# Optimization experiments

Measured on AMD Instinct MI355X. Metric: run time of the kernel, lower is better.

## Reference

```python
import jax, jax.numpy as jnp
import numpy as np
from jax import lax

P = 2048
HIDDEN = 512
NUM_STEPS = 15
BATCH = 8192
SLOPE = 25.0  # snntorch surrogate.fast_sigmoid default slope


@jax.custom_vjp
def spike_fn(x):
    # Heaviside forward, fast-sigmoid surrogate backward.
    return (x > 0).astype(x.dtype)

def _spike_fwd(x):
    return spike_fn(x), x

def _spike_bwd(x, g):
    return (g / (SLOPE * jnp.abs(x) + 1.0) ** 2,)

spike_fn.defvjp(_spike_fwd, _spike_bwd)


def setup_inputs() -> dict:
    key = jax.random.key(0)
    ks = jax.random.split(key, 6)
    x = jax.random.randint(ks[0], (BATCH, 2), 0, P)
    embed = jax.random.normal(ks[1], (P, HIDDEN), dtype=jnp.float32)
    # Linear weights stored [in, out] (transpose of torch convention, same math)
    W1 = jax.random.normal(ks[2], (2 * HIDDEN, HIDDEN), dtype=jnp.float32) * (1.0 / np.sqrt(2 * HIDDEN))
    b1 = jnp.zeros((HIDDEN,), dtype=jnp.float32)
    W2 = jax.random.normal(ks[3], (HIDDEN, P), dtype=jnp.float32) * (1.0 / np.sqrt(HIDDEN))
    b2 = jnp.zeros((P,), dtype=jnp.float32)
    beta1 = jnp.float32(0.9)
    thr1 = jnp.float32(1.0)
    beta2 = jnp.float32(0.9)
    thr2 = jnp.float32(1.0)
    return {"x": x, "embed": embed, "W1": W1, "b1": b1, "W2": W2, "b2": b2,
            "beta1": beta1, "thr1": thr1, "beta2": beta2, "thr2": thr2}


def reference(x, embed, W1, b1, W2, b2, beta1, thr1, beta2, thr2):
    # clamp params as in the torch no-grad block (identity at init values)
    beta1 = jnp.clip(beta1, 0.1, 0.9)
    beta2 = jnp.clip(beta2, 0.1, 0.9)
    thr1 = jnp.clip(thr1, 0.1, None)
    thr2 = jnp.clip(thr2, 0.1, None)

    emb = embed[x].reshape(x.shape[0], -1)          # [B, 2*hidden]
    cur1 = emb @ W1 + b1                            # constant across steps

    mem1_0 = jnp.zeros((x.shape[0], HIDDEN), dtype=jnp.float32)
    mem2_0 = jnp.zeros((x.shape[0], P), dtype=jnp.float32)

    def step(carry, _):
        mem1, mem2 = carry
        # snntorch Leaky, reset_mechanism='subtract': reset from PREVIOUS mem, detached
        reset1 = lax.stop_gradient((mem1 - thr1 > 0).astype(mem1.dtype))
        mem1 = beta1 * mem1 + cur1 - reset1 * thr1
        spk1 = spike_fn(mem1 - thr1)
        cur2 = spk1 @ W2 + b2
        # lif2 has reset_mechanism='none'
        mem2 = beta2 * mem2 + cur2
        return (mem1, mem2), None

    (mem1, mem2), _ = lax.scan(step, (mem1_0, mem2_0), None, length=NUM_STEPS)
    return mem2  # output = last mem2
```

## Files before the change

### kernel.cpp

```cpp
#include <hip/hip_runtime.h>
#include <hip/hip_bf16.h>
#include <stdint.h>

typedef float    f32x4 __attribute__((ext_vector_type(4)));
typedef _Float16 f16x4 __attribute__((ext_vector_type(4)));
typedef _Float16 f16x8 __attribute__((ext_vector_type(8)));

#define NSTEPS 15

__global__ __launch_bounds__(256) void prep_kernel(
    const float* __restrict__ embed, const float* __restrict__ W1,
    const float* __restrict__ W2,
    _Float16* __restrict__ Ap, _Float16* __restrict__ Btp,
    _Float16* __restrict__ W2T)
{
  __shared__ _Float16 sh[2][64][72];
  const int b = blockIdx.x;
  const int t = threadIdx.x;

  if (b < 1024) {
    const int i  = b * 256 + t;
    const int m  = i >> 7;
    const int k4 = (i & 127) * 4;
    f32x4 v = *(const f32x4*)&embed[(size_t)m * 512 + k4];
    f16x4 h0, h1;
#pragma unroll
    for (int j = 0; j < 4; ++j) {
      h0[j] = (_Float16)v[j];
      h1[j] = (_Float16)(v[j] - (float)h0[j]);
    }
    _Float16* r = Ap + (size_t)m * 1024 + k4;
    *(f16x4*)(r)       = h0;
    *(f16x4*)(r + 512) = h1;
  } else if (b < 1152) {
    const int idx = b - 1024;
    const int n0 = (idx & 7) * 64;
    const int k0 = ((idx >> 3) & 7) * 64;
    const int z  = idx >> 6;
    const int kk = t >> 4;
    const int n4 = (t & 15) * 4;
#pragma unroll
    for (int i = 0; i < 4; ++i) {
      f32x4 v = *(const f32x4*)&W1[(size_t)(z * 512 + k0 + kk + i * 16) * 512 + n0 + n4];
#pragma unroll
      for (int j = 0; j < 4; ++j) {
        float s = v[j] * 64.0f;
        _Float16 hi = (_Float16)s;
        sh[0][n4 + j][kk + i * 16] = hi;
        sh[1][n4 + j][kk + i * 16] = (_Float16)(s - (float)hi);
      }
    }
    __syncthreads();
#pragma unroll
    for (int i = 0; i < 2; ++i) {
      const int nn = (t >> 3) + i * 32;
      const int k8 = (t & 7) * 8;
      _Float16* r = Btp + (size_t)(z * 512 + n0 + nn) * 1024 + k0 + k8;
      *(uint4*)(r)       = *(const uint4*)&sh[0][nn][k8];
      *(uint4*)(r + 512) = *(const uint4*)&sh[1][nn][k8];
    }
  } else {
    const int idx = b - 1152;
    const int n0 = (idx & 31) * 64;
    const int k0 = (idx >> 5) * 64;
    const int kk = t >> 4;
    const int n4 = (t & 15) * 4;
#pragma unroll
    for (int i = 0; i < 4; ++i) {
      f32x4 v = *(const f32x4*)&W2[(size_t)(k0 + kk + i * 16) * 2048 + n0 + n4];
#pragma unroll
      for (int j = 0; j < 4; ++j) sh[0][n4 + j][kk + i * 16] = (_Float16)v[j];
    }
    __syncthreads();
#pragma unroll
    for (int i = 0; i < 2; ++i) {
      const int nn = (t >> 3) + i * 32;
      const int k8 = (t & 7) * 8;
      *(uint4*)&W2T[(size_t)(n0 + nn) * 512 + k0 + k8] = *(const uint4*)&sh[0][nn][k8];
    }
  }
}

__device__ __forceinline__ void gld_lds16(const void* g, void* l) {
  __builtin_amdgcn_global_load_lds(
      (const __attribute__((address_space(1))) uint32_t*)g,
      (__attribute__((address_space(3))) uint32_t*)l, 16, 0, 0);
}

__device__ __forceinline__ void g1_stage(
    const _Float16* __restrict__ Ap, const _Float16* __restrict__ Btp,
    char* lds, int m0, int n0, int wave, int lane, int tile)
{
  const int vk0  = tile * 64;
  const int acol = (vk0 < 1024) ? vk0 : vk0 - 1024;
  const int bcol = (vk0 < 1024) ? (vk0 & 511) : vk0 - 512;
  char* lb = lds + (tile % 3) * 16384;
#pragma unroll
  for (int i = 0; i < 2; ++i) {
    const int ob  = (wave * 2 + i) * 1024;
    const int o   = ob + lane * 16;
    const int row = o >> 7;
    const int c   = ((o >> 4) & 7) ^ (row & 7);
    gld_lds16(Ap + ((size_t)(m0 + row) * 1024 + acol + c * 8), lb + ob);
  }
#pragma unroll
  for (int i = 0; i < 2; ++i) {
    const int ob  = (wave * 2 + i) * 1024;
    const int o   = ob + lane * 16;
    const int row = o >> 7;
    const int c   = ((o >> 4) & 7) ^ (row & 7);
    gld_lds16(Btp + ((size_t)(n0 + row) * 1024 + bcol + c * 8), lb + 8192 + ob);
  }
}

__global__ __launch_bounds__(256) void gemm1_kernel(
    const _Float16* __restrict__ Ap,
    const _Float16* __restrict__ Btp,
    float* __restrict__ T)
{
  __shared__ __align__(16) char lds[3 * 16384];

  const int t    = threadIdx.x;
  const int lane = t & 63;
  const int wave = t >> 6;
  const int wm   = wave >> 1;
  const int wn   = wave & 1;

  int bid = blockIdx.x;
  bid = (bid & 7) * 64 + (bid >> 3);
  const int m0 = (bid >> 4) * 64;
  const int n0 = (bid & 15) * 64;

  f32x4 acc[2][2] = {};

  g1_stage(Ap, Btp, lds, m0, n0, wave, lane, 0);
  g1_stage(Ap, Btp, lds, m0, n0, wave, lane, 1);
  asm volatile("s_waitcnt vmcnt(4)" ::: "memory");
  __builtin_amdgcn_s_barrier();

  for (int kt = 0; kt < 24; ++kt) {
    const char* lb = lds + (kt % 3) * 16384;
    char* AsB = (char*)lb;
    char* BsB = (char*)lb + 8192;
    const bool pf = (kt + 2 < 24);

    f16x8 af[2][2], bf[2][2];
#pragma unroll
    for (int kk = 0; kk < 2; ++kk) {
      const int lc = (lane >> 4) + kk * 4;
#pragma unroll
      for (int mi = 0; mi < 2; ++mi) {
        const int row = wm * 32 + mi * 16 + (lane & 15);
        af[mi][kk] = *(const f16x8*)(AsB + row * 128 + ((lc ^ (row & 7)) << 4));
      }
#pragma unroll
      for (int ni = 0; ni < 2; ++ni) {
        const int row = wn * 32 + ni * 16 + (lane & 15);
        bf[ni][kk] = *(const f16x8*)(BsB + row * 128 + ((lc ^ (row & 7)) << 4));
      }
    }
    if (pf) g1_stage(Ap, Btp, lds, m0, n0, wave, lane, kt + 2);

    __builtin_amdgcn_s_setprio(1);
#pragma unroll
    for (int kk = 0; kk < 2; ++kk)
#pragma unroll
      for (int mi = 0; mi < 2; ++mi)
#pragma unroll
        for (int ni = 0; ni < 2; ++ni)
          acc[mi][ni] = __builtin_amdgcn_mfma_f32_16x16x32_f16(
              af[mi][kk], bf[ni][kk], acc[mi][ni], 0, 0, 0);
    __builtin_amdgcn_s_setprio(0);

    if (pf) asm volatile("s_waitcnt vmcnt(4)" ::: "memory");
    else    asm volatile("s_waitcnt vmcnt(0)" ::: "memory");
    __builtin_amdgcn_s_barrier();
  }

#pragma unroll
  for (int mi = 0; mi < 2; ++mi) {
    const int r0 = m0 + wm * 32 + mi * 16 + ((lane >> 4) << 2);
#pragma unroll
    for (int ni = 0; ni < 2; ++ni) {
      const int cc = n0 + wn * 32 + ni * 16 + (lane & 15);
#pragma unroll
      for (int q = 0; q < 4; ++q)
        T[(size_t)(r0 + q) * 1024 + cc] = acc[mi][ni][q] * 0.015625f;
    }
  }
}

__global__ __launch_bounds__(256) void recur_kernel(
    const int* __restrict__ x,
    const float* __restrict__ T,
    const float* __restrict__ b1,
    const float* __restrict__ beta1p, const float* __restrict__ thr1p,
    const float* __restrict__ beta2p,
    _Float16* __restrict__ S)
{
  const float beta1 = fminf(fmaxf(beta1p[0], 0.1f), 0.9f);
  const float thr1  = fmaxf(thr1p[0], 0.1f);
  const float beta2 = fminf(fmaxf(beta2p[0], 0.1f), 0.9f);

  const int t = threadIdx.x;
  const int b = blockIdx.x * 4 + (t >> 6);
  const int h = (t & 63) * 8;
  const int x0 = x[b * 2 + 0];
  const int x1 = x[b * 2 + 1];

  const float* p0 = &T[(size_t)x0 * 1024 + h];
  const float* p1 = &T[(size_t)x1 * 1024 + 512 + h];

  float cur[8];
#pragma unroll
  for (int half = 0; half < 2; ++half) {
    f32x4 a = *(const f32x4*)(p0 + half * 4);
    f32x4 c = *(const f32x4*)(p1 + half * 4);
    f32x4 e = *(const f32x4*)&b1[h + half * 4];
#pragma unroll
    for (int j = 0; j < 4; ++j)
      cur[half * 4 + j] = (a[j] + c[j]) + e[j];
  }

  float m[8] = {}, s[8] = {};
#pragma unroll
  for (int st = 0; st < NSTEPS; ++st) {
#pragma unroll
    for (int j = 0; j < 8; ++j) {
      float r = (m[j] > thr1) ? thr1 : 0.0f;
      m[j] = beta1 * m[j] + cur[j] - r;
      float sp = (m[j] > thr1) ? 1.0f : 0.0f;
      s[j] = beta2 * s[j] + sp;
    }
  }

  __align__(16) _Float16 o[8];
#pragma unroll
  for (int j = 0; j < 8; ++j) o[j] = (_Float16)s[j];
  *(uint4*)&S[(size_t)b * 512 + h] = *(const uint4*)o;
}

__device__ __forceinline__ void g2_round(
    const _Float16* __restrict__ A, const _Float16* __restrict__ Bt,
    char* lds, int m0, int n0, int wave, int lane, int tile, int r)
{
  const int k0 = tile * 64;
  char* lb = lds + (tile % 3) * 49152;
  if (r < 4) {
    const int ob  = r * 8192 + wave * 1024;
    const int o   = ob + lane * 16;
    const int row = o >> 7;
    const int c   = ((o >> 4) & 7) ^ (row & 7);
    gld_lds16(A + ((size_t)(m0 + row) * 512 + k0 + c * 8), lb + ob);
  } else {
    const int ob  = (r - 4) * 8192 + wave * 1024;
    const int o   = ob + lane * 16;
    const int row = o >> 7;
    const int c   = ((o >> 4) & 7) ^ (row & 7);
    gld_lds16(Bt + ((size_t)(n0 + row) * 512 + k0 + c * 8), lb + 32768 + ob);
  }
}

template<int QA>
__device__ __forceinline__ void g2_mfma16(
    f32x4 (&acc)[8][2], const f16x8 (&af)[4][2], const f16x8 (&bf)[2][2])
{
#pragma unroll
  for (int kk = 0; kk < 2; ++kk)
#pragma unroll
    for (int mi = 0; mi < 4; ++mi)
#pragma unroll
      for (int ni = 0; ni < 2; ++ni)
        acc[QA * 4 + mi][ni] = __builtin_amdgcn_mfma_f32_16x16x32_f16(
            af[mi][kk], bf[ni][kk], acc[QA * 4 + mi][ni], 0, 0, 0);
}

template<int QA>
__device__ __forceinline__ void g2_lda(
    f16x8 (&af)[4][2], const char* lb, int wm, int lane)
{
#pragma unroll
  for (int mi = 0; mi < 4; ++mi) {
    const int row = wm * 128 + QA * 64 + mi * 16 + (lane & 15);
#pragma unroll
    for (int kk = 0; kk < 2; ++kk) {
      const int lc = (lane >> 4) + kk * 4;
      af[mi][kk] = *(const f16x8*)(lb + row * 128 + ((lc ^ (row & 7)) << 4));
    }
  }
}

__device__ __forceinline__ void g2_ldb(
    f16x8 (&bf)[2][2], const char* lb, int wn, int lane)
{
#pragma unroll
  for (int ni = 0; ni < 2; ++ni) {
    const int row = wn * 32 + ni * 16 + (lane & 15);
#pragma unroll
    for (int kk = 0; kk < 2; ++kk) {
      const int lc = (lane >> 4) + kk * 4;
      bf[ni][kk] = *(const f16x8*)(lb + 32768 + row * 128 + ((lc ^ (row & 7)) << 4));
    }
  }
}

__global__ __launch_bounds__(512, 2) void gemm2_pipe_kernel(
    const _Float16* __restrict__ A,
    const _Float16* __restrict__ Bt,
    const float* __restrict__ b2,
    const float* __restrict__ beta2p,
    float* __restrict__ C)
{
  __shared__ __align__(16) char lds[3 * 49152];

  const int t    = threadIdx.x;
  const int lane = t & 63;
  const int wave = t >> 6;
  const int wm   = wave >> 2;
  const int wn   = wave & 3;

  int bid = blockIdx.x;
  bid = (bid & 7) * 64 + (bid >> 3);
  const int m0 = (bid >> 4) * 256;
  const int n0 = (bid & 15) * 128;

  f32x4 acc[8][2] = {};
  f16x8 af[4][2], bf[2][2];

#pragma unroll
  for (int r = 0; r < 6; ++r) g2_round(A, Bt, lds, m0, n0, wave, lane, 0, r);
#pragma unroll
  for (int r = 0; r < 6; ++r) g2_round(A, Bt, lds, m0, n0, wave, lane, 1, r);
  asm volatile("s_waitcnt vmcnt(6)" ::: "memory");
  __builtin_amdgcn_s_barrier();

  for (int tt = 0; tt < 8; ++tt) {
    const char* lb = lds + (tt % 3) * 49152;
    const bool pf = (tt + 2 < 8);

    g2_lda<0>(af, lb, wm, lane);
    g2_ldb(bf, lb, wn, lane);
    if (pf) {
      g2_round(A, Bt, lds, m0, n0, wave, lane, tt + 2, 0);
      g2_round(A, Bt, lds, m0, n0, wave, lane, tt + 2, 1);
      g2_round(A, Bt, lds, m0, n0, wave, lane, tt + 2, 2);
    }
    __builtin_amdgcn_s_barrier();
    asm volatile("s_waitcnt lgkmcnt(0)" ::: "memory");
    __builtin_amdgcn_s_setprio(1);
    g2_mfma16<0>(acc, af, bf);
    __builtin_amdgcn_s_setprio(0);
    __builtin_amdgcn_s_barrier();

    g2_lda<1>(af, lb, wm, lane);
    if (pf) {
      g2_round(A, Bt, lds, m0, n0, wave, lane, tt + 2, 3);
      g2_round(A, Bt, lds, m0, n0, wave, lane, tt + 2, 4);
      g2_round(A, Bt, lds, m0, n0, wave, lane, tt + 2, 5);
    }
    __builtin_amdgcn_s_barrier();
    asm volatile("s_waitcnt lgkmcnt(0)" ::: "memory");
    __builtin_amdgcn_s_setprio(1);
    g2_mfma16<1>(acc, af, bf);
    __builtin_amdgcn_s_setprio(0);
    asm volatile("s_waitcnt vmcnt(6)" ::: "memory");
    __builtin_amdgcn_s_barrier();
  }

  const float beta2 = fminf(fmaxf(beta2p[0], 0.1f), 0.9f);
  float cb = 0.0f;
  for (int i = 0; i < NSTEPS; ++i) cb = beta2 * cb + 1.0f;

#pragma unroll
  for (int a = 0; a < 8; ++a) {
    const int r0 = m0 + wm * 128 + a * 16 + ((lane >> 4) << 2);
#pragma unroll
    for (int ni = 0; ni < 2; ++ni) {
      const int cc = n0 + wn * 32 + ni * 16 + (lane & 15);
      const float bv = cb * b2[cc];
#pragma unroll
      for (int q = 0; q < 4; ++q)
        C[(size_t)(r0 + q) * 2048 + cc] = acc[a][ni][q] + bv;
    }
  }
}

extern "C" void kernel_launch(void* const* d_in, const int* in_sizes, int n_in,
                              void* d_out, int out_size, void* d_ws, size_t ws_size,
                              hipStream_t stream) {
  const int*   x     = (const int*)  d_in[0];
  const float* embed = (const float*)d_in[1];
  const float* W1    = (const float*)d_in[2];
  const float* b1    = (const float*)d_in[3];
  const float* W2    = (const float*)d_in[4];
  const float* b2    = (const float*)d_in[5];
  const float* beta1 = (const float*)d_in[6];
  const float* thr1  = (const float*)d_in[7];
  const float* beta2 = (const float*)d_in[8];
  float* out = (float*)d_out;

  char* ws = (char*)d_ws;
  float*    T   = (float*)   ws;
  _Float16* Ap  = (_Float16*)(ws + ( 8u << 20));
  _Float16* Btp = (_Float16*)(ws + (12u << 20));
  _Float16* W2T = (_Float16*)(ws + (14u << 20));
  _Float16* S   = (_Float16*)(ws + (16u << 20));

  prep_kernel<<<dim3(1408), 256, 0, stream>>>(embed, W1, W2, Ap, Btp, W2T);

  gemm1_kernel<<<dim3(512), 256, 0, stream>>>(Ap, Btp, T);

  recur_kernel<<<dim3(2048), 256, 0, stream>>>(x, T, b1, beta1, thr1, beta2, S);

  gemm2_pipe_kernel<<<dim3(512), 512, 0, stream>>>(S, W2T, b2, beta2, out);
}
```

Measured before the change: 64.42 us.

## Shrink GEMM2 K-tile to 32 with 4x2 wave grid and higher occupancy

Restructures the second GEMM pipeline to use K-tiles of 32 instead of 64, halving LDS per stage so four blocks can fit per CU (launch bounds 512,4). The wave layout changes from 2x4 with 128x32 per wave to 4x2 with 64x64 per wave. Each iteration now has a single barrier and a single prefetch stage, where before the two half-iterations were interleaved. The block-to-XCD mapping is also rewritten so each XCD covers a contiguous M range. This trades deeper per-tile work and more barriers per K for lower LDS use, higher occupancy and better operand reuse per wave.

```diff
diff --git a/kernel.cpp b/kernel.cpp
--- a/kernel.cpp
+++ b/kernel.cpp
@@ -240,130 +240,86 @@
   *(uint4*)&S[(size_t)b * 512 + h] = *(const uint4*)o;
 }
 
-__device__ __forceinline__ void g2_round(
+__device__ __forceinline__ void g2_stage(
     const _Float16* __restrict__ A, const _Float16* __restrict__ Bt,
-    char* lds, int m0, int n0, int wave, int lane, int tile, int r)
-{
-  const int k0 = tile * 64;
-  char* lb = lds + (tile % 3) * 49152;
-  if (r < 4) {
-    const int ob  = r * 8192 + wave * 1024;
+    char* lds, int m0, int n0, int wave, int lane, int tile)
+{
+  const int k0 = tile * 32;
+  char* lb = lds + (tile % 3) * 24576;
+#pragma unroll
+  for (int i = 0; i < 2; ++i) {
+    const int ob  = i * 8192 + wave * 1024;
     const int o   = ob + lane * 16;
-    const int row = o >> 7;
-    const int c   = ((o >> 4) & 7) ^ (row & 7);
+    const int row = o >> 6;
+    const int c   = ((o >> 4) & 3) ^ ((row >> 1) & 3);
     gld_lds16(A + ((size_t)(m0 + row) * 512 + k0 + c * 8), lb + ob);
-  } else {
-    const int ob  = (r - 4) * 8192 + wave * 1024;
+  }
+  {
+    const int ob  = wave * 1024;
     const int o   = ob + lane * 16;
-    const int row = o >> 7;
-    const int c   = ((o >> 4) & 7) ^ (row & 7);
-    gld_lds16(Bt + ((size_t)(n0 + row) * 512 + k0 + c * 8), lb + 32768 + ob);
-  }
-}
-
-template<int QA>
-__device__ __forceinline__ void g2_mfma16(
-    f32x4 (&acc)[8][2], const f16x8 (&af)[4][2], const f16x8 (&bf)[2][2])
-{
-#pragma unroll
-  for (int kk = 0; kk < 2; ++kk)
-#pragma unroll
-    for (int mi = 0; mi < 4; ++mi)
-#pragma unroll
-      for (int ni = 0; ni < 2; ++ni)
-        acc[QA * 4 + mi][ni] = __builtin_amdgcn_mfma_f32_16x16x32_f16(
-            af[mi][kk], bf[ni][kk], acc[QA * 4 + mi][ni], 0, 0, 0);
-}
-
-template<int QA>
-__device__ __forceinline__ void g2_lda(
-    f16x8 (&af)[4][2], const char* lb, int wm, int lane)
-{
-#pragma unroll
-  for (int mi = 0; mi < 4; ++mi) {
-    const int row = wm * 128 + QA * 64 + mi * 16 + (lane & 15);
-#pragma unroll
-    for (int kk = 0; kk < 2; ++kk) {
-      const int lc = (lane >> 4) + kk * 4;
-      af[mi][kk] = *(const f16x8*)(lb + row * 128 + ((lc ^ (row & 7)) << 4));
-    }
-  }
-}
-
-__device__ __forceinline__ void g2_ldb(
-    f16x8 (&bf)[2][2], const char* lb, int wn, int lane)
-{
-#pragma unroll
-  for (int ni = 0; ni < 2; ++ni) {
-    const int row = wn * 32 + ni * 16 + (lane & 15);
-#pragma unroll
-    for (int kk = 0; kk < 2; ++kk) {
-      const int lc = (lane >> 4) + kk * 4;
-      bf[ni][kk] = *(const f16x8*)(lb + 32768 + row * 128 + ((lc ^ (row & 7)) << 4));
-    }
-  }
-}
-
-__global__ __launch_bounds__(512, 2) void gemm2_pipe_kernel(
+    const int row = o >> 6;
+    const int c   = ((o >> 4) & 3) ^ ((row >> 1) & 3);
+    gld_lds16(Bt + ((size_t)(n0 + row) * 512 + k0 + c * 8), lb + 16384 + ob);
+  }
+}
+
+__global__ __launch_bounds__(512, 4) void gemm2_pipe_kernel(
     const _Float16* __restrict__ A,
     const _Float16* __restrict__ Bt,
     const float* __restrict__ b2,
     const float* __restrict__ beta2p,
     float* __restrict__ C)
 {
-  __shared__ __align__(16) char lds[3 * 49152];
+  __shared__ __align__(16) char lds[3 * 24576];
 
   const int t    = threadIdx.x;
   const int lane = t & 63;
   const int wave = t >> 6;
-  const int wm   = wave >> 2;
-  const int wn   = wave & 3;
-
-  int bid = blockIdx.x;
-  bid = (bid & 7) * 64 + (bid >> 3);
-  const int m0 = (bid >> 4) * 256;
-  const int n0 = (bid & 15) * 128;
-
-  f32x4 acc[8][2] = {};
-  f16x8 af[4][2], bf[2][2];
-
-#pragma unroll
-  for (int r = 0; r < 6; ++r) g2_round(A, Bt, lds, m0, n0, wave, lane, 0, r);
-#pragma unroll
-  for (int r = 0; r < 6; ++r) g2_round(A, Bt, lds, m0, n0, wave, lane, 1, r);
-  asm volatile("s_waitcnt vmcnt(6)" ::: "memory");
+  const int wm   = wave >> 1;
+  const int wn   = wave & 1;
+
+  const int bid = blockIdx.x;
+  const int xcd = bid & 7;
+  const int j   = bid >> 3;
+  const int m0  = (xcd * 4 + (j >> 4)) * 256;
+  const int n0  = (j & 15) * 128;
+
+  f32x4 acc[4][4] = {};
+
+  g2_stage(A, Bt, lds, m0, n0, wave, lane, 0);
+  g2_stage(A, Bt, lds, m0, n0, wave, lane, 1);
+  asm volatile("s_waitcnt vmcnt(3)" ::: "memory");
   __builtin_amdgcn_s_barrier();
 
-  for (int tt = 0; tt < 8; ++tt) {
-    const char* lb = lds + (tt % 3) * 49152;
-    const bool pf = (tt + 2 < 8);
-
-    g2_lda<0>(af, lb, wm, lane);
-    g2_ldb(bf, lb, wn, lane);
-    if (pf) {
-      g2_round(A, Bt, lds, m0, n0, wave, lane, tt + 2, 0);
-      g2_round(A, Bt, lds, m0, n0, wave, lane, tt + 2, 1);
-      g2_round(A, Bt, lds, m0, n0, wave, lane, tt + 2, 2);
-    }
-    __builtin_amdgcn_s_barrier();
-    asm volatile("s_waitcnt lgkmcnt(0)" ::: "memory");
+  for (int kt = 0; kt < 16; ++kt) {
+    const char* lb = lds + (kt % 3) * 24576;
+    const bool pf = (kt + 2 < 16);
+
+    const int lc = lane >> 4;
+    f16x8 af[4], bf[4];
+#pragma unroll
+    for (int mi = 0; mi < 4; ++mi) {
+      const int row = wm * 64 + mi * 16 + (lane & 15);
+      af[mi] = *(const f16x8*)(lb + row * 64 + ((lc ^ ((row >> 1) & 3)) << 4));
+    }
+#pragma unroll
+    for (int ni = 0; ni < 4; ++ni) {
+      const int row = wn * 64 + ni * 16 + (lane & 15);
+      bf[ni] = *(const f16x8*)(lb + 16384 + row * 64 + ((lc ^ ((row >> 1) & 3)) << 4));
+    }
+    if (pf) g2_stage(A, Bt, lds, m0, n0, wave, lane, kt + 2);
+
     __builtin_amdgcn_s_setprio(1);
-    g2_mfma16<0>(acc, af, bf);
+#pragma unroll
+    for (int mi = 0; mi < 4; ++mi)
+#pragma unroll
+      for (int ni = 0; ni < 4; ++ni)
+        acc[mi][ni] = __builtin_amdgcn_mfma_f32_16x16x32_f16(
+            af[mi], bf[ni], acc[mi][ni], 0, 0, 0);
     __builtin_amdgcn_s_setprio(0);
-    __builtin_amdgcn_s_barrier();
-
-    g2_lda<1>(af, lb, wm, lane);
-    if (pf) {
-      g2_round(A, Bt, lds, m0, n0, wave, lane, tt + 2, 3);
-      g2_round(A, Bt, lds, m0, n0, wave, lane, tt + 2, 4);
-      g2_round(A, Bt, lds, m0, n0, wave, lane, tt + 2, 5);
-    }
-    __builtin_amdgcn_s_barrier();
-    asm volatile("s_waitcnt lgkmcnt(0)" ::: "memory");
-    __builtin_amdgcn_s_setprio(1);
-    g2_mfma16<1>(acc, af, bf);
-    __builtin_amdgcn_s_setprio(0);
-    asm volatile("s_waitcnt vmcnt(6)" ::: "memory");
+
+    if (pf) asm volatile("s_waitcnt vmcnt(3)" ::: "memory");
+    else    asm volatile("s_waitcnt vmcnt(0)" ::: "memory");
     __builtin_amdgcn_s_barrier();
   }
 
@@ -372,15 +328,15 @@
   for (int i = 0; i < NSTEPS; ++i) cb = beta2 * cb + 1.0f;
 
 #pragma unroll
-  for (int a = 0; a < 8; ++a) {
-    const int r0 = m0 + wm * 128 + a * 16 + ((lane >> 4) << 2);
-#pragma unroll
-    for (int ni = 0; ni < 2; ++ni) {
-      const int cc = n0 + wn * 32 + ni * 16 + (lane & 15);
+  for (int mi = 0; mi < 4; ++mi) {
+    const int r0 = m0 + wm * 64 + mi * 16 + ((lane >> 4) << 2);
+#pragma unroll
+    for (int ni = 0; ni < 4; ++ni) {
+      const int cc = n0 + wn * 64 + ni * 16 + (lane & 15);
       const float bv = cb * b2[cc];
 #pragma unroll
       for (int q = 0; q < 4; ++q)
-        C[(size_t)(r0 + q) * 2048 + cc] = acc[a][ni][q] + bv;
+        C[(size_t)(r0 + q) * 2048 + cc] = acc[mi][ni][q] + bv;
     }
   }
 }
```

New measurement: 63.75 us. Within noise of the previous version (-1.0%).
